# Kernel tuning notes

Hardware: AMD Instinct MI355X
Metric: run time of the kernel (lower is better)

Reference implementation:

```python
import jax, jax.numpy as jnp
import numpy as np

# Static segment boundaries: lengths [512,512,512] + remainder -> ranges below
SEG_RANGES = [(0, 512), (512, 1024), (1024, 1536), (1536, 2048)]

B, N, D, H = 8, 2048, 1024, 2048
NUM_SEG = len(SEG_RANGES)


def setup_inputs() -> dict:
    key = jax.random.key(0)
    k_x, k1, k2, k3 = jax.random.split(key, 4)
    scale_in = 1.0 / np.sqrt(D)
    scale_h = 1.0 / np.sqrt(H)
    return {
        "x": jax.random.normal(k_x, (B, N, D), dtype=jnp.float32),
        "w1": jax.random.normal(k1, (NUM_SEG, D, H), dtype=jnp.float32) * scale_in,
        "w3": jax.random.normal(k2, (NUM_SEG, D, H), dtype=jnp.float32) * scale_in,
        "w2": jax.random.normal(k3, (NUM_SEG, H, D), dtype=jnp.float32) * scale_h,
    }


def reference(x, w1, w3, w2):
    # Per-segment independent SwiGLU FFN: out_seg = (silu(x W1) * (x W3)) W2
    outs = []
    for i, (s, e) in enumerate(SEG_RANGES):
        seg = jax.lax.dynamic_slice_in_dim(x, s, e - s, axis=-2)  # [B, L_i, D]
        h = jax.nn.silu(jnp.einsum('bld,dh->blh', seg, w1[i])) \
            * jnp.einsum('bld,dh->blh', seg, w3[i])               # [B, L_i, H]
        outs.append(jnp.einsum('blh,hd->bld', h, w2[i]))          # [B, L_i, D]
    # Segments tile [0, N) exactly, so concat == the .at[s:e].set() scatter loop
    return jnp.concatenate(outs, axis=-2)
```

## Files before the change

kernel.cpp:

```cpp
#include <hip/hip_runtime.h>
#include <hip/hip_bf16.h>

typedef __bf16 bf16_t;
typedef __attribute__((ext_vector_type(8))) __bf16 bf16x8;
typedef __attribute__((ext_vector_type(4))) float f32x4;
typedef __attribute__((ext_vector_type(8))) unsigned short ushort8v;

#define MFMA16(a, b, c) __builtin_amdgcn_mfma_f32_16x16x32_bf16((a), (b), (c), 0, 0, 0)
#define BC8(x) __builtin_bit_cast(bf16x8, (x))

__device__ __forceinline__ unsigned short f2bf(float f) {
    bf16_t b = (bf16_t)f;
    return __builtin_bit_cast(unsigned short, b);
}

__device__ __forceinline__ void gload16(const void* g, void* l) {
    __builtin_amdgcn_global_load_lds(
        (const __attribute__((address_space(1))) void*)g,
        (__attribute__((address_space(3))) void*)l,
        16, 0, 0);
}

__global__ __launch_bounds__(256) void cvtx(const float* __restrict__ src,
                                            bf16_t* __restrict__ dst) {
    size_t i = ((size_t)blockIdx.x * 256 + threadIdx.x) * 8;
    f32x4 v0 = *(const f32x4*)(src + i);
    f32x4 v1 = *(const f32x4*)(src + i + 4);
    bf16x8 o;
    o[0] = (bf16_t)v0[0]; o[1] = (bf16_t)v0[1];
    o[2] = (bf16_t)v0[2]; o[3] = (bf16_t)v0[3];
    o[4] = (bf16_t)v1[0]; o[5] = (bf16_t)v1[1];
    o[6] = (bf16_t)v1[2]; o[7] = (bf16_t)v1[3];
    *(bf16x8*)(dst + i) = o;
}

__global__ __launch_bounds__(256) void transcvt64(const float* __restrict__ src,
                                                  unsigned short* __restrict__ dst,
                                                  int R, int C) {
    __shared__ __align__(16) unsigned short tile[64][66];
    size_t off = (size_t)blockIdx.z * R * C;
    const float* s = src + off;
    unsigned short* d = dst + off;
    int tr = blockIdx.y * 64, tc = blockIdx.x * 64;
    int tid = threadIdx.x;
    int lr = tid >> 4;
    int lc = (tid & 15) * 4;
#pragma unroll
    for (int p = 0; p < 4; ++p) {
        int r = p * 16 + lr;
        f32x4 v = *(const f32x4*)(s + (size_t)(tr + r) * C + tc + lc);
        tile[r][lc + 0] = f2bf(v[0]); tile[r][lc + 1] = f2bf(v[1]);
        tile[r][lc + 2] = f2bf(v[2]); tile[r][lc + 3] = f2bf(v[3]);
    }
    __syncthreads();
#pragma unroll
    for (int q = 0; q < 2; ++q) {
        int item = q * 256 + tid;
        int oc = item >> 3;
        int rb = (item & 7) * 8;
        ushort8v v;
#pragma unroll
        for (int t = 0; t < 8; ++t) v[t] = tile[rb + t][oc];
        *(ushort8v*)(d + (size_t)(tc + oc) * R + tr + rb) = v;
    }
}


#define PH_FENCE __builtin_amdgcn_sched_barrier(0)
#define LGKMN(n) { asm volatile("s_waitcnt lgkmcnt(" #n ")" ::: "memory"); \
                   __builtin_amdgcn_sched_barrier(0); }
#define VMW(n) asm volatile("s_waitcnt vmcnt(" #n ")" ::: "memory")
#define DSR(dst, a, OFF) asm volatile("ds_read_b128 %0, %1 " OFF : "=v"(dst) : "v"(a))

__global__ __launch_bounds__(512, 2) void gemm13(const bf16_t* __restrict__ Xb,
                                                 const bf16_t* __restrict__ W1t,
                                                 const bf16_t* __restrict__ W3t,
                                                 bf16_t* __restrict__ Hh,
                                                 int row_base) {
    const int K = 1024, N = 2048;
    int nwg = gridDim.x, id = blockIdx.x;
    if ((nwg & 7) == 0) id = (id & 7) * (nwg >> 3) + (id >> 3);
    int nbx = nwg >> 4;
    int bx = id % nbx, by = id / nbx;
    int row0 = bx * 256, col0 = by * 128;
    int seg = ((row_base + row0) & 2047) >> 9;
    const bf16_t* Ag  = Xb + (size_t)row0 * K;
    const bf16_t* B1g = W1t + ((size_t)seg * N + col0) * K;
    const bf16_t* B3g = W3t + ((size_t)seg * N + col0) * K;

    __shared__ __align__(16) bf16_t smem[65536];

    int tid = threadIdx.x, lane = tid & 63, w = tid >> 6;
    int wm = w >> 1, wn = w & 1;
    int quad = lane >> 4, l16 = lane & 15;

    int r0 = 2 * (tid >> 3) + ((tid >> 2) & 1);
    int c0 = (tid & 3) ^ ((tid >> 3) & 3);
    int offG  = r0 * K + c0 * 8;
    int offG2 = offG + 128 * K;

    int sigRd = ((l16 & 1) << 2) | (quad ^ ((l16 >> 1) & 3));
    int rdAB = ((wm * 32 + (l16 >> 1)) * 64 + sigRd * 8) * 2;
    int rdBB = ((wn * 32 + (l16 >> 1)) * 64 + sigRd * 8) * 2;

    f32x4 accU[4][4], accV[4][4];
    f32x4 z = {0.f, 0.f, 0.f, 0.f};
#pragma unroll
    for (int i = 0; i < 4; ++i)
#pragma unroll
        for (int j = 0; j < 4; ++j) { accU[i][j] = z; accV[i][j] = z; }

    f32x4 af[4], bU[4], bV[4];

#define STG13(slot, hh) { bf16_t* d_ = smem + (slot) * 16384; const int kg_ = (hh) * 32; \
    gload16(Ag + kg_ + offG,  d_ + tid * 8); \
    gload16(Ag + kg_ + offG2, d_ + 4096 + tid * 8); \
    gload16(B1g + kg_ + offG, d_ + 8192 + tid * 8); \
    gload16(B3g + kg_ + offG, d_ + 12288 + tid * 8); }

#define HALF13(slot, STG, WAIT) {                                               \
    PH_FENCE;                                                                   \
    STG;                                                                        \
    int aA_ = (slot) * 32768 + rdAB;                                            \
    int aB_ = (slot) * 32768 + rdBB;                                            \
    DSR(af[0], aA_, "offset:0");     DSR(af[1], aA_, "offset:1024");            \
    DSR(af[2], aA_, "offset:2048");  DSR(af[3], aA_, "offset:3072");            \
    DSR(bU[0], aB_, "offset:16384"); DSR(bU[1], aB_, "offset:17408");           \
    DSR(bU[2], aB_, "offset:18432"); DSR(bU[3], aB_, "offset:19456");           \
    DSR(bV[0], aB_, "offset:24576"); DSR(bV[1], aB_, "offset:25600");           \
    DSR(bV[2], aB_, "offset:26624"); DSR(bV[3], aB_, "offset:27648");           \
    LGKMN(4);                                                                   \
    __builtin_amdgcn_s_setprio(1);                                              \
    _Pragma("unroll")                                                           \
    for (int i_ = 0; i_ < 4; ++i_)                                              \
        _Pragma("unroll")                                                       \
        for (int j_ = 0; j_ < 4; ++j_)                                          \
            accU[i_][j_] = MFMA16(BC8(af[i_]), BC8(bU[j_]), accU[i_][j_]);      \
    __builtin_amdgcn_s_setprio(0);                                              \
    LGKMN(0);                                                                   \
    __builtin_amdgcn_s_setprio(1);                                              \
    _Pragma("unroll")                                                           \
    for (int i_ = 0; i_ < 4; ++i_)                                              \
        _Pragma("unroll")                                                       \
        for (int j_ = 0; j_ < 4; ++j_)                                          \
            accV[i_][j_] = MFMA16(BC8(af[i_]), BC8(bV[j_]), accV[i_][j_]);      \
    __builtin_amdgcn_s_setprio(0);                                              \
    WAIT;                                                                       \
    __builtin_amdgcn_s_barrier(); }

    STG13(0, 0); STG13(1, 1); STG13(2, 2);
    VMW(8);
    __builtin_amdgcn_s_barrier();

#pragma unroll 1
    for (int h = 0; h < 28; h += 4) {
        HALF13(0, STG13(3, h + 3), VMW(8));
        HALF13(1, STG13(0, h + 4), VMW(8));
        HALF13(2, STG13(1, h + 5), VMW(8));
        HALF13(3, STG13(2, h + 6), VMW(8));
    }
    HALF13(0, STG13(3, 31), VMW(8));
    HALF13(1, , VMW(4));
    HALF13(2, , VMW(0));
    HALF13(3, , );

    __syncthreads();
    bf16_t* Ct = smem;
#pragma unroll
    for (int i = 0; i < 4; ++i)
#pragma unroll
        for (int j = 0; j < 4; ++j) {
            int r = wm * 64 + i * 16 + quad * 4;
            int c = wn * 64 + j * 16 + l16;
#pragma unroll
            for (int t = 0; t < 4; ++t) {
                float u = accU[i][j][t];
                float v = accV[i][j][t];
                float h = (u / (1.f + __expf(-u))) * v;
                Ct[(r + t) * 136 + c] = (bf16_t)h;
            }
        }
    __syncthreads();
#pragma unroll
    for (int s = 0; s < 8; ++s) {
        int r = s * 32 + (tid >> 4);
        int cb = (tid & 15) * 8;
        bf16x8 v = *(const bf16x8*)(Ct + r * 136 + cb);
        *(bf16x8*)(Hh + (size_t)(row0 + r) * N + col0 + cb) = v;
    }
#undef HALF13
#undef STG13
}

__global__ __launch_bounds__(512, 2) void gemm2k(const bf16_t* __restrict__ Hh,
                                                 const bf16_t* __restrict__ W2t,
                                                 float* __restrict__ Outc,
                                                 int row_base) {
    const int K = 2048, N = 1024;
    int nwg = gridDim.x, id = blockIdx.x;
    if ((nwg & 7) == 0) id = (id & 7) * (nwg >> 3) + (id >> 3);
    int nbx = nwg >> 2;
    int bx = id % nbx, by = id / nbx;
    int row0 = bx * 256, col0 = by * 256;
    int seg = ((row_base + row0) & 2047) >> 9;
    const bf16_t* Ag = Hh + (size_t)row0 * K;
    const bf16_t* Bg = W2t + ((size_t)seg * N + col0) * K;

    __shared__ __align__(16) bf16_t smem[65536];

    int tid = threadIdx.x, lane = tid & 63, w = tid >> 6;
    int wm = w >> 2, wn = w & 3;
    int quad = lane >> 4, l16 = lane & 15;

    int r0 = 2 * (tid >> 3) + ((tid >> 2) & 1);
    int c0 = (tid & 3) ^ ((tid >> 3) & 3);
    int offG  = r0 * K + c0 * 8;
    int offG2 = offG + 128 * K;

    int sigRd = ((l16 & 1) << 2) | (quad ^ ((l16 >> 1) & 3));
    int rdAB = ((wm * 64 + (l16 >> 1)) * 64 + sigRd * 8) * 2;
    int rdBB = ((wn * 32 + (l16 >> 1)) * 64 + sigRd * 8) * 2;

    f32x4 acc[8][4];
    f32x4 z = {0.f, 0.f, 0.f, 0.f};
#pragma unroll
    for (int i = 0; i < 8; ++i)
#pragma unroll
        for (int j = 0; j < 4; ++j) acc[i][j] = z;

    f32x4 af[4], ag[4], bfr[4];

#define STG2(slot, hh) { bf16_t* d_ = smem + (slot) * 16384; const int kg_ = (hh) * 32; \
    gload16(Ag + kg_ + offG,  d_ + tid * 8); \
    gload16(Ag + kg_ + offG2, d_ + 4096 + tid * 8); \
    gload16(Bg + kg_ + offG,  d_ + 8192 + tid * 8); \
    gload16(Bg + kg_ + offG2, d_ + 12288 + tid * 8); }

#define HALF2(slot, STG, WAIT) {                                                \
    PH_FENCE;                                                                   \
    STG;                                                                        \
    int aA_ = (slot) * 32768 + rdAB;                                            \
    int aB_ = (slot) * 32768 + rdBB;                                            \
    DSR(af[0], aA_, "offset:0");      DSR(af[1], aA_, "offset:1024");           \
    DSR(af[2], aA_, "offset:2048");   DSR(af[3], aA_, "offset:3072");           \
    DSR(bfr[0], aB_, "offset:16384"); DSR(bfr[1], aB_, "offset:17408");         \
    DSR(bfr[2], aB_, "offset:18432"); DSR(bfr[3], aB_, "offset:19456");         \
    DSR(ag[0], aA_, "offset:4096");   DSR(ag[1], aA_, "offset:5120");           \
    DSR(ag[2], aA_, "offset:6144");   DSR(ag[3], aA_, "offset:7168");           \
    LGKMN(4);                                                                   \
    __builtin_amdgcn_s_setprio(1);                                              \
    _Pragma("unroll")                                                           \
    for (int i_ = 0; i_ < 4; ++i_)                                              \
        _Pragma("unroll")                                                       \
        for (int j_ = 0; j_ < 4; ++j_)                                          \
            acc[i_][j_] = MFMA16(BC8(af[i_]), BC8(bfr[j_]), acc[i_][j_]);       \
    __builtin_amdgcn_s_setprio(0);                                              \
    LGKMN(0);                                                                   \
    __builtin_amdgcn_s_setprio(1);                                              \
    _Pragma("unroll")                                                           \
    for (int i_ = 0; i_ < 4; ++i_)                                              \
        _Pragma("unroll")                                                       \
        for (int j_ = 0; j_ < 4; ++j_)                                          \
            acc[4 + i_][j_] = MFMA16(BC8(ag[i_]), BC8(bfr[j_]), acc[4 + i_][j_]); \
    __builtin_amdgcn_s_setprio(0);                                              \
    WAIT;                                                                       \
    __builtin_amdgcn_s_barrier(); }

    STG2(0, 0); STG2(1, 1); STG2(2, 2);
    VMW(8);
    __builtin_amdgcn_s_barrier();

#pragma unroll 1
    for (int h = 0; h < 60; h += 4) {
        HALF2(0, STG2(3, h + 3), VMW(8));
        HALF2(1, STG2(0, h + 4), VMW(8));
        HALF2(2, STG2(1, h + 5), VMW(8));
        HALF2(3, STG2(2, h + 6), VMW(8));
    }
    HALF2(0, STG2(3, 63), VMW(8));
    HALF2(1, , VMW(4));
    HALF2(2, , VMW(0));
    HALF2(3, , );

    __syncthreads();
    float* smemf = (float*)smem;
    for (int pass = 0; pass < 4; ++pass) {
        if (pass) __syncthreads();
        if (wm == (pass >> 1)) {
            int mq = pass & 1;
#pragma unroll
            for (int i = 0; i < 4; ++i)
#pragma unroll
                for (int j = 0; j < 4; ++j) {
                    int r = i * 16 + quad * 4;
                    int c = wn * 64 + j * 16 + l16;
#pragma unroll
                    for (int t = 0; t < 4; ++t)
                        smemf[(r + t) * 260 + c] = acc[mq * 4 + i][j][t];
                }
        }
        __syncthreads();
#pragma unroll
        for (int s = 0; s < 8; ++s) {
            int r = s * 8 + w;
            f32x4 v = *(const f32x4*)(smemf + r * 260 + lane * 4);
            *(f32x4*)(Outc + (size_t)(row0 + pass * 64 + r) * N + col0 + lane * 4) = v;
        }
    }
#undef HALF2
#undef STG2
}

extern "C" void kernel_launch(void* const* d_in, const int* in_sizes, int n_in,
                              void* d_out, int out_size, void* d_ws, size_t ws_size,
                              hipStream_t stream) {
    const float* x  = (const float*)d_in[0];
    const float* w1 = (const float*)d_in[1];
    const float* w3 = (const float*)d_in[2];
    const float* w2 = (const float*)d_in[3];
    float* out = (float*)d_out;

    const size_t WSEG = (size_t)4 * 1024 * 2048;
    bf16_t* w1t = (bf16_t*)d_ws;
    bf16_t* w3t = w1t + WSEG;
    bf16_t* w2t = w3t + WSEG;
    bf16_t* dyn = w2t + WSEG;

    transcvt64<<<dim3(32, 16, 4), 256, 0, stream>>>(w1, (unsigned short*)w1t, 1024, 2048);
    transcvt64<<<dim3(32, 16, 4), 256, 0, stream>>>(w3, (unsigned short*)w3t, 1024, 2048);
    transcvt64<<<dim3(16, 32, 4), 256, 0, stream>>>(w2, (unsigned short*)w2t, 2048, 1024);

    const int TOTAL_ROWS = 16384;
    size_t wbytes = 3 * WSEG * sizeof(bf16_t);
    size_t avail = (ws_size > wbytes) ? ws_size - wbytes : 0;
    int chunk_rows = TOTAL_ROWS;
    while (chunk_rows > 256 && (size_t)chunk_rows * 6144 > avail)
        chunk_rows >>= 1;

    for (int rb = 0; rb < TOTAL_ROWS; rb += chunk_rows) {
        bf16_t* Xb = dyn;
        bf16_t* Hh = dyn + (size_t)chunk_rows * 1024;
        cvtx<<<chunk_rows / 2, 256, 0, stream>>>(x + (size_t)rb * 1024, Xb);
        gemm13<<<(chunk_rows / 256) * 16, 512, 0, stream>>>(Xb, w1t, w3t, Hh, rb);
        gemm2k<<<(chunk_rows / 256) * 4, 512, 0, stream>>>(Hh, w2t, out + (size_t)rb * 1024, rb);
    }
}
```

Before: 400.3 us.

## Double-buffer LDS fragment registers to prefetch next stage during MFMAs

```diff
diff --git a/kernel.cpp b/kernel.cpp
--- a/kernel.cpp
+++ b/kernel.cpp
@@ -66,7 +66,6 @@
 }
 
 
-#define PH_FENCE __builtin_amdgcn_sched_barrier(0)
 #define LGKMN(n) { asm volatile("s_waitcnt lgkmcnt(" #n ")" ::: "memory"); \
                    __builtin_amdgcn_sched_barrier(0); }
 #define VMW(n) asm volatile("s_waitcnt vmcnt(" #n ")" ::: "memory")
@@ -110,7 +109,7 @@
 #pragma unroll
         for (int j = 0; j < 4; ++j) { accU[i][j] = z; accV[i][j] = z; }
 
-    f32x4 af[4], bU[4], bV[4];
+    f32x4 af[2][4], bU[2][4], bV[2][4];
 
 #define STG13(slot, hh) { bf16_t* d_ = smem + (slot) * 16384; const int kg_ = (hh) * 32; \
     gload16(Ag + kg_ + offG,  d_ + tid * 8); \
@@ -118,51 +117,52 @@
     gload16(B1g + kg_ + offG, d_ + 8192 + tid * 8); \
     gload16(B3g + kg_ + offG, d_ + 12288 + tid * 8); }
 
-#define HALF13(slot, STG, WAIT) {                                               \
-    PH_FENCE;                                                                   \
+#define RD13(slotN, BN) {                                                       \
+    int aA_ = (slotN) * 32768 + rdAB;                                           \
+    int aB_ = (slotN) * 32768 + rdBB;                                           \
+    DSR(af[BN][0], aA_, "offset:0");     DSR(af[BN][1], aA_, "offset:1024");    \
+    DSR(af[BN][2], aA_, "offset:2048");  DSR(af[BN][3], aA_, "offset:3072");    \
+    DSR(bU[BN][0], aB_, "offset:16384"); DSR(bU[BN][1], aB_, "offset:17408");   \
+    DSR(bU[BN][2], aB_, "offset:18432"); DSR(bU[BN][3], aB_, "offset:19456");   \
+    DSR(bV[BN][0], aB_, "offset:24576"); DSR(bV[BN][1], aB_, "offset:25600");   \
+    DSR(bV[BN][2], aB_, "offset:26624"); DSR(bV[BN][3], aB_, "offset:27648"); }
+
+#define HALF13(BC, RD, STG, WAIT) {                                             \
+    LGKMN(0);                                                                   \
+    RD;                                                                         \
     STG;                                                                        \
-    int aA_ = (slot) * 32768 + rdAB;                                            \
-    int aB_ = (slot) * 32768 + rdBB;                                            \
-    DSR(af[0], aA_, "offset:0");     DSR(af[1], aA_, "offset:1024");            \
-    DSR(af[2], aA_, "offset:2048");  DSR(af[3], aA_, "offset:3072");            \
-    DSR(bU[0], aB_, "offset:16384"); DSR(bU[1], aB_, "offset:17408");           \
-    DSR(bU[2], aB_, "offset:18432"); DSR(bU[3], aB_, "offset:19456");           \
-    DSR(bV[0], aB_, "offset:24576"); DSR(bV[1], aB_, "offset:25600");           \
-    DSR(bV[2], aB_, "offset:26624"); DSR(bV[3], aB_, "offset:27648");           \
-    LGKMN(4);                                                                   \
+    __builtin_amdgcn_sched_barrier(0);                                          \
     __builtin_amdgcn_s_setprio(1);                                              \
     _Pragma("unroll")                                                           \
     for (int i_ = 0; i_ < 4; ++i_)                                              \
         _Pragma("unroll")                                                       \
         for (int j_ = 0; j_ < 4; ++j_)                                          \
-            accU[i_][j_] = MFMA16(BC8(af[i_]), BC8(bU[j_]), accU[i_][j_]);      \
-    __builtin_amdgcn_s_setprio(0);                                              \
-    LGKMN(0);                                                                   \
-    __builtin_amdgcn_s_setprio(1);                                              \
+            accU[i_][j_] = MFMA16(BC8(af[BC][i_]), BC8(bU[BC][j_]), accU[i_][j_]); \
     _Pragma("unroll")                                                           \
     for (int i_ = 0; i_ < 4; ++i_)                                              \
         _Pragma("unroll")                                                       \
         for (int j_ = 0; j_ < 4; ++j_)                                          \
-            accV[i_][j_] = MFMA16(BC8(af[i_]), BC8(bV[j_]), accV[i_][j_]);      \
+            accV[i_][j_] = MFMA16(BC8(af[BC][i_]), BC8(bV[BC][j_]), accV[i_][j_]); \
     __builtin_amdgcn_s_setprio(0);                                              \
     WAIT;                                                                       \
     __builtin_amdgcn_s_barrier(); }
 
     STG13(0, 0); STG13(1, 1); STG13(2, 2);
-    VMW(8);
+    VMW(4);
     __builtin_amdgcn_s_barrier();
+    RD13(0, 0);
 
 #pragma unroll 1
     for (int h = 0; h < 28; h += 4) {
-        HALF13(0, STG13(3, h + 3), VMW(8));
-        HALF13(1, STG13(0, h + 4), VMW(8));
-        HALF13(2, STG13(1, h + 5), VMW(8));
-        HALF13(3, STG13(2, h + 6), VMW(8));
-    }
-    HALF13(0, STG13(3, 31), VMW(8));
-    HALF13(1, , VMW(4));
-    HALF13(2, , VMW(0));
-    HALF13(3, , );
+        HALF13(0, RD13(1, 1), STG13(3, h + 3), VMW(4));
+        HALF13(1, RD13(2, 0), STG13(0, h + 4), VMW(4));
+        HALF13(0 + 0, RD13(3, 1), STG13(1, h + 5), VMW(4));
+        HALF13(1, RD13(0, 0), STG13(2, h + 6), VMW(4));
+    }
+    HALF13(0, RD13(1, 1), STG13(3, 31), VMW(4));
+    HALF13(1, RD13(2, 0), , VMW(0));
+    HALF13(0, RD13(3, 1), , );
+    HALF13(1, , , );
 
     __syncthreads();
     bf16_t* Ct = smem;
@@ -189,6 +189,7 @@
         *(bf16x8*)(Hh + (size_t)(row0 + r) * N + col0 + cb) = v;
     }
 #undef HALF13
+#undef RD13
 #undef STG13
 }
 
@@ -228,7 +229,7 @@
 #pragma unroll
         for (int j = 0; j < 4; ++j) acc[i][j] = z;
 
-    f32x4 af[4], ag[4], bfr[4];
+    f32x4 af[2][4], ag[2][4], bfr[2][4];
 
 #define STG2(slot, hh) { bf16_t* d_ = smem + (slot) * 16384; const int kg_ = (hh) * 32; \
     gload16(Ag + kg_ + offG,  d_ + tid * 8); \
@@ -236,51 +237,52 @@
     gload16(Bg + kg_ + offG,  d_ + 8192 + tid * 8); \
     gload16(Bg + kg_ + offG2, d_ + 12288 + tid * 8); }
 
-#define HALF2(slot, STG, WAIT) {                                                \
-    PH_FENCE;                                                                   \
+#define RD2(slotN, BN) {                                                        \
+    int aA_ = (slotN) * 32768 + rdAB;                                           \
+    int aB_ = (slotN) * 32768 + rdBB;                                           \
+    DSR(af[BN][0], aA_, "offset:0");      DSR(af[BN][1], aA_, "offset:1024");   \
+    DSR(af[BN][2], aA_, "offset:2048");   DSR(af[BN][3], aA_, "offset:3072");   \
+    DSR(ag[BN][0], aA_, "offset:4096");   DSR(ag[BN][1], aA_, "offset:5120");   \
+    DSR(ag[BN][2], aA_, "offset:6144");   DSR(ag[BN][3], aA_, "offset:7168");   \
+    DSR(bfr[BN][0], aB_, "offset:16384"); DSR(bfr[BN][1], aB_, "offset:17408"); \
+    DSR(bfr[BN][2], aB_, "offset:18432"); DSR(bfr[BN][3], aB_, "offset:19456"); }
+
+#define HALF2(BC, RD, STG, WAIT) {                                              \
+    LGKMN(0);                                                                   \
+    RD;                                                                         \
     STG;                                                                        \
-    int aA_ = (slot) * 32768 + rdAB;                                            \
-    int aB_ = (slot) * 32768 + rdBB;                                            \
-    DSR(af[0], aA_, "offset:0");      DSR(af[1], aA_, "offset:1024");           \
-    DSR(af[2], aA_, "offset:2048");   DSR(af[3], aA_, "offset:3072");           \
-    DSR(bfr[0], aB_, "offset:16384"); DSR(bfr[1], aB_, "offset:17408");         \
-    DSR(bfr[2], aB_, "offset:18432"); DSR(bfr[3], aB_, "offset:19456");         \
-    DSR(ag[0], aA_, "offset:4096");   DSR(ag[1], aA_, "offset:5120");           \
-    DSR(ag[2], aA_, "offset:6144");   DSR(ag[3], aA_, "offset:7168");           \
-    LGKMN(4);                                                                   \
+    __builtin_amdgcn_sched_barrier(0);                                          \
     __builtin_amdgcn_s_setprio(1);                                              \
     _Pragma("unroll")                                                           \
     for (int i_ = 0; i_ < 4; ++i_)                                              \
         _Pragma("unroll")                                                       \
         for (int j_ = 0; j_ < 4; ++j_)                                          \
-            acc[i_][j_] = MFMA16(BC8(af[i_]), BC8(bfr[j_]), acc[i_][j_]);       \
-    __builtin_amdgcn_s_setprio(0);                                              \
-    LGKMN(0);                                                                   \
-    __builtin_amdgcn_s_setprio(1);                                              \
+            acc[i_][j_] = MFMA16(BC8(af[BC][i_]), BC8(bfr[BC][j_]), acc[i_][j_]); \
     _Pragma("unroll")                                                           \
     for (int i_ = 0; i_ < 4; ++i_)                                              \
         _Pragma("unroll")                                                       \
         for (int j_ = 0; j_ < 4; ++j_)                                          \
-            acc[4 + i_][j_] = MFMA16(BC8(ag[i_]), BC8(bfr[j_]), acc[4 + i_][j_]); \
+            acc[4 + i_][j_] = MFMA16(BC8(ag[BC][i_]), BC8(bfr[BC][j_]), acc[4 + i_][j_]); \
     __builtin_amdgcn_s_setprio(0);                                              \
     WAIT;                                                                       \
     __builtin_amdgcn_s_barrier(); }
 
     STG2(0, 0); STG2(1, 1); STG2(2, 2);
-    VMW(8);
+    VMW(4);
     __builtin_amdgcn_s_barrier();
+    RD2(0, 0);
 
 #pragma unroll 1
     for (int h = 0; h < 60; h += 4) {
-        HALF2(0, STG2(3, h + 3), VMW(8));
-        HALF2(1, STG2(0, h + 4), VMW(8));
-        HALF2(2, STG2(1, h + 5), VMW(8));
-        HALF2(3, STG2(2, h + 6), VMW(8));
-    }
-    HALF2(0, STG2(3, 63), VMW(8));
-    HALF2(1, , VMW(4));
-    HALF2(2, , VMW(0));
-    HALF2(3, , );
+        HALF2(0, RD2(1, 1), STG2(3, h + 3), VMW(4));
+        HALF2(1, RD2(2, 0), STG2(0, h + 4), VMW(4));
+        HALF2(0, RD2(3, 1), STG2(1, h + 5), VMW(4));
+        HALF2(1, RD2(0, 0), STG2(2, h + 6), VMW(4));
+    }
+    HALF2(0, RD2(1, 1), STG2(3, 63), VMW(4));
+    HALF2(1, RD2(2, 0), , VMW(0));
+    HALF2(0, RD2(3, 1), , );
+    HALF2(1, , , );
 
     __syncthreads();
     float* smemf = (float*)smem;
@@ -308,6 +310,7 @@
         }
     }
 #undef HALF2
+#undef RD2
 #undef STG2
 }
 
```

Measured after the change: 592.1 us. +47.9%, slower.

## Split each K-step into two barrier-separated phases interleaving loads and MFMA

Applied to the files above, without the earlier changes.

```diff
diff --git a/kernel.cpp b/kernel.cpp
--- a/kernel.cpp
+++ b/kernel.cpp
@@ -66,7 +66,6 @@
 }
 
 
-#define PH_FENCE __builtin_amdgcn_sched_barrier(0)
 #define LGKMN(n) { asm volatile("s_waitcnt lgkmcnt(" #n ")" ::: "memory"); \
                    __builtin_amdgcn_sched_barrier(0); }
 #define VMW(n) asm volatile("s_waitcnt vmcnt(" #n ")" ::: "memory")
@@ -112,24 +111,23 @@
 
     f32x4 af[4], bU[4], bV[4];
 
-#define STG13(slot, hh) { bf16_t* d_ = smem + (slot) * 16384; const int kg_ = (hh) * 32; \
+#define STGA13(slot, hh) { bf16_t* d_ = smem + (slot) * 16384; const int kg_ = (hh) * 32; \
     gload16(Ag + kg_ + offG,  d_ + tid * 8); \
-    gload16(Ag + kg_ + offG2, d_ + 4096 + tid * 8); \
+    gload16(Ag + kg_ + offG2, d_ + 4096 + tid * 8); }
+#define STGB13(slot, hh) { bf16_t* d_ = smem + (slot) * 16384; const int kg_ = (hh) * 32; \
     gload16(B1g + kg_ + offG, d_ + 8192 + tid * 8); \
     gload16(B3g + kg_ + offG, d_ + 12288 + tid * 8); }
 
-#define HALF13(slot, STG, WAIT) {                                               \
-    PH_FENCE;                                                                   \
-    STG;                                                                        \
+#define PHA13(slot, STG) {                                                      \
     int aA_ = (slot) * 32768 + rdAB;                                            \
     int aB_ = (slot) * 32768 + rdBB;                                            \
     DSR(af[0], aA_, "offset:0");     DSR(af[1], aA_, "offset:1024");            \
     DSR(af[2], aA_, "offset:2048");  DSR(af[3], aA_, "offset:3072");            \
     DSR(bU[0], aB_, "offset:16384"); DSR(bU[1], aB_, "offset:17408");           \
     DSR(bU[2], aB_, "offset:18432"); DSR(bU[3], aB_, "offset:19456");           \
-    DSR(bV[0], aB_, "offset:24576"); DSR(bV[1], aB_, "offset:25600");           \
-    DSR(bV[2], aB_, "offset:26624"); DSR(bV[3], aB_, "offset:27648");           \
-    LGKMN(4);                                                                   \
+    STG;                                                                        \
+    __builtin_amdgcn_s_barrier();                                               \
+    LGKMN(0);                                                                   \
     __builtin_amdgcn_s_setprio(1);                                              \
     _Pragma("unroll")                                                           \
     for (int i_ = 0; i_ < 4; ++i_)                                              \
@@ -137,6 +135,15 @@
         for (int j_ = 0; j_ < 4; ++j_)                                          \
             accU[i_][j_] = MFMA16(BC8(af[i_]), BC8(bU[j_]), accU[i_][j_]);      \
     __builtin_amdgcn_s_setprio(0);                                              \
+    __builtin_amdgcn_s_barrier(); }
+
+#define PHB13(slot, STG, WAIT) {                                                \
+    int aB_ = (slot) * 32768 + rdBB;                                            \
+    DSR(bV[0], aB_, "offset:24576"); DSR(bV[1], aB_, "offset:25600");           \
+    DSR(bV[2], aB_, "offset:26624"); DSR(bV[3], aB_, "offset:27648");           \
+    STG;                                                                        \
+    WAIT;                                                                       \
+    __builtin_amdgcn_s_barrier();                                               \
     LGKMN(0);                                                                   \
     __builtin_amdgcn_s_setprio(1);                                              \
     _Pragma("unroll")                                                           \
@@ -145,24 +152,25 @@
         for (int j_ = 0; j_ < 4; ++j_)                                          \
             accV[i_][j_] = MFMA16(BC8(af[i_]), BC8(bV[j_]), accV[i_][j_]);      \
     __builtin_amdgcn_s_setprio(0);                                              \
-    WAIT;                                                                       \
     __builtin_amdgcn_s_barrier(); }
 
-    STG13(0, 0); STG13(1, 1); STG13(2, 2);
+    STGA13(0, 0); STGB13(0, 0);
+    STGA13(1, 1); STGB13(1, 1);
+    STGA13(2, 2); STGB13(2, 2);
     VMW(8);
     __builtin_amdgcn_s_barrier();
 
 #pragma unroll 1
     for (int h = 0; h < 28; h += 4) {
-        HALF13(0, STG13(3, h + 3), VMW(8));
-        HALF13(1, STG13(0, h + 4), VMW(8));
-        HALF13(2, STG13(1, h + 5), VMW(8));
-        HALF13(3, STG13(2, h + 6), VMW(8));
-    }
-    HALF13(0, STG13(3, 31), VMW(8));
-    HALF13(1, , VMW(4));
-    HALF13(2, , VMW(0));
-    HALF13(3, , );
+        PHA13(0, STGA13(3, h + 3)); PHB13(0, STGB13(3, h + 3), VMW(8));
+        PHA13(1, STGA13(0, h + 4)); PHB13(1, STGB13(0, h + 4), VMW(8));
+        PHA13(2, STGA13(1, h + 5)); PHB13(2, STGB13(1, h + 5), VMW(8));
+        PHA13(3, STGA13(2, h + 6)); PHB13(3, STGB13(2, h + 6), VMW(8));
+    }
+    PHA13(0, STGA13(3, 31)); PHB13(0, STGB13(3, 31), VMW(8));
+    PHA13(1, );              PHB13(1, , VMW(4));
+    PHA13(2, );              PHB13(2, , VMW(0));
+    PHA13(3, );              PHB13(3, , );
 
     __syncthreads();
     bf16_t* Ct = smem;
@@ -188,8 +196,10 @@
         bf16x8 v = *(const bf16x8*)(Ct + r * 136 + cb);
         *(bf16x8*)(Hh + (size_t)(row0 + r) * N + col0 + cb) = v;
     }
-#undef HALF13
-#undef STG13
+#undef PHA13
+#undef PHB13
+#undef STGA13
+#undef STGB13
 }
 
 __global__ __launch_bounds__(512, 2) void gemm2k(const bf16_t* __restrict__ Hh,
@@ -230,24 +240,23 @@
 
     f32x4 af[4], ag[4], bfr[4];
 
-#define STG2(slot, hh) { bf16_t* d_ = smem + (slot) * 16384; const int kg_ = (hh) * 32; \
+#define STGA2(slot, hh) { bf16_t* d_ = smem + (slot) * 16384; const int kg_ = (hh) * 32; \
     gload16(Ag + kg_ + offG,  d_ + tid * 8); \
-    gload16(Ag + kg_ + offG2, d_ + 4096 + tid * 8); \
+    gload16(Ag + kg_ + offG2, d_ + 4096 + tid * 8); }
+#define STGB2(slot, hh) { bf16_t* d_ = smem + (slot) * 16384; const int kg_ = (hh) * 32; \
     gload16(Bg + kg_ + offG,  d_ + 8192 + tid * 8); \
     gload16(Bg + kg_ + offG2, d_ + 12288 + tid * 8); }
 
-#define HALF2(slot, STG, WAIT) {                                                \
-    PH_FENCE;                                                                   \
-    STG;                                                                        \
+#define PHA2(slot, STG) {                                                       \
     int aA_ = (slot) * 32768 + rdAB;                                            \
     int aB_ = (slot) * 32768 + rdBB;                                            \
     DSR(af[0], aA_, "offset:0");      DSR(af[1], aA_, "offset:1024");           \
     DSR(af[2], aA_, "offset:2048");   DSR(af[3], aA_, "offset:3072");           \
     DSR(bfr[0], aB_, "offset:16384"); DSR(bfr[1], aB_, "offset:17408");         \
     DSR(bfr[2], aB_, "offset:18432"); DSR(bfr[3], aB_, "offset:19456");         \
-    DSR(ag[0], aA_, "offset:4096");   DSR(ag[1], aA_, "offset:5120");           \
-    DSR(ag[2], aA_, "offset:6144");   DSR(ag[3], aA_, "offset:7168");           \
-    LGKMN(4);                                                                   \
+    STG;                                                                        \
+    __builtin_amdgcn_s_barrier();                                               \
+    LGKMN(0);                                                                   \
     __builtin_amdgcn_s_setprio(1);                                              \
     _Pragma("unroll")                                                           \
     for (int i_ = 0; i_ < 4; ++i_)                                              \
@@ -255,6 +264,15 @@
         for (int j_ = 0; j_ < 4; ++j_)                                          \
             acc[i_][j_] = MFMA16(BC8(af[i_]), BC8(bfr[j_]), acc[i_][j_]);       \
     __builtin_amdgcn_s_setprio(0);                                              \
+    __builtin_amdgcn_s_barrier(); }
+
+#define PHB2(slot, STG, WAIT) {                                                 \
+    int aA_ = (slot) * 32768 + rdAB;                                            \
+    DSR(ag[0], aA_, "offset:4096");   DSR(ag[1], aA_, "offset:5120");           \
+    DSR(ag[2], aA_, "offset:6144");   DSR(ag[3], aA_, "offset:7168");           \
+    STG;                                                                        \
+    WAIT;                                                                       \
+    __builtin_amdgcn_s_barrier();                                               \
     LGKMN(0);                                                                   \
     __builtin_amdgcn_s_setprio(1);                                              \
     _Pragma("unroll")                                                           \
@@ -263,24 +281,25 @@
         for (int j_ = 0; j_ < 4; ++j_)                                          \
             acc[4 + i_][j_] = MFMA16(BC8(ag[i_]), BC8(bfr[j_]), acc[4 + i_][j_]); \
     __builtin_amdgcn_s_setprio(0);                                              \
-    WAIT;                                                                       \
     __builtin_amdgcn_s_barrier(); }
 
-    STG2(0, 0); STG2(1, 1); STG2(2, 2);
+    STGA2(0, 0); STGB2(0, 0);
+    STGA2(1, 1); STGB2(1, 1);
+    STGA2(2, 2); STGB2(2, 2);
     VMW(8);
     __builtin_amdgcn_s_barrier();
 
 #pragma unroll 1
     for (int h = 0; h < 60; h += 4) {
-        HALF2(0, STG2(3, h + 3), VMW(8));
-        HALF2(1, STG2(0, h + 4), VMW(8));
-        HALF2(2, STG2(1, h + 5), VMW(8));
-        HALF2(3, STG2(2, h + 6), VMW(8));
-    }
-    HALF2(0, STG2(3, 63), VMW(8));
-    HALF2(1, , VMW(4));
-    HALF2(2, , VMW(0));
-    HALF2(3, , );
+        PHA2(0, STGA2(3, h + 3)); PHB2(0, STGB2(3, h + 3), VMW(8));
+        PHA2(1, STGA2(0, h + 4)); PHB2(1, STGB2(0, h + 4), VMW(8));
+        PHA2(2, STGA2(1, h + 5)); PHB2(2, STGB2(1, h + 5), VMW(8));
+        PHA2(3, STGA2(2, h + 6)); PHB2(3, STGB2(2, h + 6), VMW(8));
+    }
+    PHA2(0, STGA2(3, 63)); PHB2(0, STGB2(3, 63), VMW(8));
+    PHA2(1, );             PHB2(1, , VMW(4));
+    PHA2(2, );             PHB2(2, , VMW(0));
+    PHA2(3, );             PHB2(3, , );
 
     __syncthreads();
     float* smemf = (float*)smem;
@@ -307,8 +326,10 @@
             *(f32x4*)(Outc + (size_t)(row0 + pass * 64 + r) * N + col0 + lane * 4) = v;
         }
     }
-#undef HALF2
-#undef STG2
+#undef PHA2
+#undef PHB2
+#undef STGA2
+#undef STGB2
 }
 
 extern "C" void kernel_launch(void* const* d_in, const int* in_sizes, int n_in,
```

Result: no change. 403.0 us (+0.7%).

## Shrink GEMM workgroups to 256 threads with 128-row tiles and triple buffering

Applied to the files above, without the earlier changes.

```diff
diff --git a/kernel.cpp b/kernel.cpp
--- a/kernel.cpp
+++ b/kernel.cpp
@@ -66,13 +66,12 @@
 }
 
 
-#define PH_FENCE __builtin_amdgcn_sched_barrier(0)
 #define LGKMN(n) { asm volatile("s_waitcnt lgkmcnt(" #n ")" ::: "memory"); \
                    __builtin_amdgcn_sched_barrier(0); }
 #define VMW(n) asm volatile("s_waitcnt vmcnt(" #n ")" ::: "memory")
 #define DSR(dst, a, OFF) asm volatile("ds_read_b128 %0, %1 " OFF : "=v"(dst) : "v"(a))
 
-__global__ __launch_bounds__(512, 2) void gemm13(const bf16_t* __restrict__ Xb,
+__global__ __launch_bounds__(256, 2) void gemm13(const bf16_t* __restrict__ Xb,
                                                  const bf16_t* __restrict__ W1t,
                                                  const bf16_t* __restrict__ W3t,
                                                  bf16_t* __restrict__ Hh,
@@ -82,13 +81,13 @@
     if ((nwg & 7) == 0) id = (id & 7) * (nwg >> 3) + (id >> 3);
     int nbx = nwg >> 4;
     int bx = id % nbx, by = id / nbx;
-    int row0 = bx * 256, col0 = by * 128;
+    int row0 = bx * 128, col0 = by * 128;
     int seg = ((row_base + row0) & 2047) >> 9;
     const bf16_t* Ag  = Xb + (size_t)row0 * K;
     const bf16_t* B1g = W1t + ((size_t)seg * N + col0) * K;
     const bf16_t* B3g = W3t + ((size_t)seg * N + col0) * K;
 
-    __shared__ __align__(16) bf16_t smem[65536];
+    __shared__ __align__(16) bf16_t smem[36864];
 
     int tid = threadIdx.x, lane = tid & 63, w = tid >> 6;
     int wm = w >> 1, wn = w & 1;
@@ -96,8 +95,7 @@
 
     int r0 = 2 * (tid >> 3) + ((tid >> 2) & 1);
     int c0 = (tid & 3) ^ ((tid >> 3) & 3);
-    int offG  = r0 * K + c0 * 8;
-    int offG2 = offG + 128 * K;
+    int offG = r0 * K + c0 * 8;
 
     int sigRd = ((l16 & 1) << 2) | (quad ^ ((l16 >> 1) & 3));
     int rdAB = ((wm * 32 + (l16 >> 1)) * 64 + sigRd * 8) * 2;
@@ -112,23 +110,24 @@
 
     f32x4 af[4], bU[4], bV[4];
 
-#define STG13(slot, hh) { bf16_t* d_ = smem + (slot) * 16384; const int kg_ = (hh) * 32; \
-    gload16(Ag + kg_ + offG,  d_ + tid * 8); \
-    gload16(Ag + kg_ + offG2, d_ + 4096 + tid * 8); \
-    gload16(B1g + kg_ + offG, d_ + 8192 + tid * 8); \
-    gload16(B3g + kg_ + offG, d_ + 12288 + tid * 8); }
+#define STG13(slot, hh) { bf16_t* d_ = smem + (slot) * 12288; const int kg_ = (hh) * 32; \
+    gload16(Ag + kg_ + offG,          d_ + tid * 8); \
+    gload16(Ag + kg_ + offG + 65536,  d_ + 2048 + tid * 8); \
+    gload16(B1g + kg_ + offG,         d_ + 4096 + tid * 8); \
+    gload16(B1g + kg_ + offG + 65536, d_ + 6144 + tid * 8); \
+    gload16(B3g + kg_ + offG,         d_ + 8192 + tid * 8); \
+    gload16(B3g + kg_ + offG + 65536, d_ + 10240 + tid * 8); }
 
 #define HALF13(slot, STG, WAIT) {                                               \
-    PH_FENCE;                                                                   \
+    int aA_ = (slot) * 24576 + rdAB;                                            \
+    int aB_ = (slot) * 24576 + 8192 + rdBB;                                     \
+    DSR(af[0], aA_, "offset:0");    DSR(af[1], aA_, "offset:1024");             \
+    DSR(af[2], aA_, "offset:2048"); DSR(af[3], aA_, "offset:3072");             \
+    DSR(bU[0], aB_, "offset:0");    DSR(bU[1], aB_, "offset:1024");             \
+    DSR(bU[2], aB_, "offset:2048"); DSR(bU[3], aB_, "offset:3072");             \
+    DSR(bV[0], aB_, "offset:8192"); DSR(bV[1], aB_, "offset:9216");             \
+    DSR(bV[2], aB_, "offset:10240");DSR(bV[3], aB_, "offset:11264");            \
     STG;                                                                        \
-    int aA_ = (slot) * 32768 + rdAB;                                            \
-    int aB_ = (slot) * 32768 + rdBB;                                            \
-    DSR(af[0], aA_, "offset:0");     DSR(af[1], aA_, "offset:1024");            \
-    DSR(af[2], aA_, "offset:2048");  DSR(af[3], aA_, "offset:3072");            \
-    DSR(bU[0], aB_, "offset:16384"); DSR(bU[1], aB_, "offset:17408");           \
-    DSR(bU[2], aB_, "offset:18432"); DSR(bU[3], aB_, "offset:19456");           \
-    DSR(bV[0], aB_, "offset:24576"); DSR(bV[1], aB_, "offset:25600");           \
-    DSR(bV[2], aB_, "offset:26624"); DSR(bV[3], aB_, "offset:27648");           \
     LGKMN(4);                                                                   \
     __builtin_amdgcn_s_setprio(1);                                              \
     _Pragma("unroll")                                                           \
@@ -148,21 +147,21 @@
     WAIT;                                                                       \
     __builtin_amdgcn_s_barrier(); }
 
-    STG13(0, 0); STG13(1, 1); STG13(2, 2);
-    VMW(8);
+    STG13(0, 0); STG13(1, 1);
+    VMW(6);
     __builtin_amdgcn_s_barrier();
 
 #pragma unroll 1
-    for (int h = 0; h < 28; h += 4) {
-        HALF13(0, STG13(3, h + 3), VMW(8));
-        HALF13(1, STG13(0, h + 4), VMW(8));
-        HALF13(2, STG13(1, h + 5), VMW(8));
-        HALF13(3, STG13(2, h + 6), VMW(8));
-    }
-    HALF13(0, STG13(3, 31), VMW(8));
-    HALF13(1, , VMW(4));
-    HALF13(2, , VMW(0));
-    HALF13(3, , );
+    for (int h = 0; h < 27; h += 3) {
+        HALF13(0, STG13(2, h + 2), VMW(6));
+        HALF13(1, STG13(0, h + 3), VMW(6));
+        HALF13(2, STG13(1, h + 4), VMW(6));
+    }
+    HALF13(0, STG13(2, 29), VMW(6));
+    HALF13(1, STG13(0, 30), VMW(6));
+    HALF13(2, STG13(1, 31), VMW(6));
+    HALF13(0, , VMW(0));
+    HALF13(1, , );
 
     __syncthreads();
     bf16_t* Ct = smem;
@@ -183,7 +182,7 @@
     __syncthreads();
 #pragma unroll
     for (int s = 0; s < 8; ++s) {
-        int r = s * 32 + (tid >> 4);
+        int r = s * 16 + (tid >> 4);
         int cb = (tid & 15) * 8;
         bf16x8 v = *(const bf16x8*)(Ct + r * 136 + cb);
         *(bf16x8*)(Hh + (size_t)(row0 + r) * N + col0 + cb) = v;
@@ -192,7 +191,7 @@
 #undef STG13
 }
 
-__global__ __launch_bounds__(512, 2) void gemm2k(const bf16_t* __restrict__ Hh,
+__global__ __launch_bounds__(256, 2) void gemm2k(const bf16_t* __restrict__ Hh,
                                                  const bf16_t* __restrict__ W2t,
                                                  float* __restrict__ Outc,
                                                  int row_base) {
@@ -201,52 +200,52 @@
     if ((nwg & 7) == 0) id = (id & 7) * (nwg >> 3) + (id >> 3);
     int nbx = nwg >> 2;
     int bx = id % nbx, by = id / nbx;
-    int row0 = bx * 256, col0 = by * 256;
+    int row0 = bx * 128, col0 = by * 256;
     int seg = ((row_base + row0) & 2047) >> 9;
     const bf16_t* Ag = Hh + (size_t)row0 * K;
     const bf16_t* Bg = W2t + ((size_t)seg * N + col0) * K;
 
-    __shared__ __align__(16) bf16_t smem[65536];
+    __shared__ __align__(16) bf16_t smem[36864];
 
     int tid = threadIdx.x, lane = tid & 63, w = tid >> 6;
-    int wm = w >> 2, wn = w & 3;
+    int wm = w >> 1, wn = w & 1;
     int quad = lane >> 4, l16 = lane & 15;
 
     int r0 = 2 * (tid >> 3) + ((tid >> 2) & 1);
     int c0 = (tid & 3) ^ ((tid >> 3) & 3);
-    int offG  = r0 * K + c0 * 8;
-    int offG2 = offG + 128 * K;
+    int offG = r0 * K + c0 * 8;
 
     int sigRd = ((l16 & 1) << 2) | (quad ^ ((l16 >> 1) & 3));
-    int rdAB = ((wm * 64 + (l16 >> 1)) * 64 + sigRd * 8) * 2;
-    int rdBB = ((wn * 32 + (l16 >> 1)) * 64 + sigRd * 8) * 2;
-
-    f32x4 acc[8][4];
+    int rdAB = ((wm * 32 + (l16 >> 1)) * 64 + sigRd * 8) * 2;
+    int rdBB = ((wn * 64 + (l16 >> 1)) * 64 + sigRd * 8) * 2;
+
+    f32x4 acc[4][8];
     f32x4 z = {0.f, 0.f, 0.f, 0.f};
 #pragma unroll
-    for (int i = 0; i < 8; ++i)
-#pragma unroll
-        for (int j = 0; j < 4; ++j) acc[i][j] = z;
-
-    f32x4 af[4], ag[4], bfr[4];
-
-#define STG2(slot, hh) { bf16_t* d_ = smem + (slot) * 16384; const int kg_ = (hh) * 32; \
-    gload16(Ag + kg_ + offG,  d_ + tid * 8); \
-    gload16(Ag + kg_ + offG2, d_ + 4096 + tid * 8); \
-    gload16(Bg + kg_ + offG,  d_ + 8192 + tid * 8); \
-    gload16(Bg + kg_ + offG2, d_ + 12288 + tid * 8); }
+    for (int i = 0; i < 4; ++i)
+#pragma unroll
+        for (int j = 0; j < 8; ++j) acc[i][j] = z;
+
+    f32x4 af[4], bfr[8];
+
+#define STG2(slot, hh) { bf16_t* d_ = smem + (slot) * 12288; const int kg_ = (hh) * 32; \
+    gload16(Ag + kg_ + offG,           d_ + tid * 8); \
+    gload16(Ag + kg_ + offG + 131072,  d_ + 2048 + tid * 8); \
+    gload16(Bg + kg_ + offG,           d_ + 4096 + tid * 8); \
+    gload16(Bg + kg_ + offG + 131072,  d_ + 6144 + tid * 8); \
+    gload16(Bg + kg_ + offG + 262144,  d_ + 8192 + tid * 8); \
+    gload16(Bg + kg_ + offG + 393216,  d_ + 10240 + tid * 8); }
 
 #define HALF2(slot, STG, WAIT) {                                                \
-    PH_FENCE;                                                                   \
+    int aA_ = (slot) * 24576 + rdAB;                                            \
+    int aB_ = (slot) * 24576 + 8192 + rdBB;                                     \
+    DSR(af[0], aA_, "offset:0");     DSR(af[1], aA_, "offset:1024");            \
+    DSR(af[2], aA_, "offset:2048");  DSR(af[3], aA_, "offset:3072");            \
+    DSR(bfr[0], aB_, "offset:0");    DSR(bfr[1], aB_, "offset:1024");           \
+    DSR(bfr[2], aB_, "offset:2048"); DSR(bfr[3], aB_, "offset:3072");           \
+    DSR(bfr[4], aB_, "offset:4096"); DSR(bfr[5], aB_, "offset:5120");           \
+    DSR(bfr[6], aB_, "offset:6144"); DSR(bfr[7], aB_, "offset:7168");           \
     STG;                                                                        \
-    int aA_ = (slot) * 32768 + rdAB;                                            \
-    int aB_ = (slot) * 32768 + rdBB;                                            \
-    DSR(af[0], aA_, "offset:0");      DSR(af[1], aA_, "offset:1024");           \
-    DSR(af[2], aA_, "offset:2048");   DSR(af[3], aA_, "offset:3072");           \
-    DSR(bfr[0], aB_, "offset:16384"); DSR(bfr[1], aB_, "offset:17408");         \
-    DSR(bfr[2], aB_, "offset:18432"); DSR(bfr[3], aB_, "offset:19456");         \
-    DSR(ag[0], aA_, "offset:4096");   DSR(ag[1], aA_, "offset:5120");           \
-    DSR(ag[2], aA_, "offset:6144");   DSR(ag[3], aA_, "offset:7168");           \
     LGKMN(4);                                                                   \
     __builtin_amdgcn_s_setprio(1);                                              \
     _Pragma("unroll")                                                           \
@@ -261,50 +260,49 @@
     for (int i_ = 0; i_ < 4; ++i_)                                              \
         _Pragma("unroll")                                                       \
         for (int j_ = 0; j_ < 4; ++j_)                                          \
-            acc[4 + i_][j_] = MFMA16(BC8(ag[i_]), BC8(bfr[j_]), acc[4 + i_][j_]); \
+            acc[i_][4 + j_] = MFMA16(BC8(af[i_]), BC8(bfr[4 + j_]), acc[i_][4 + j_]); \
     __builtin_amdgcn_s_setprio(0);                                              \
     WAIT;                                                                       \
     __builtin_amdgcn_s_barrier(); }
 
-    STG2(0, 0); STG2(1, 1); STG2(2, 2);
-    VMW(8);
+    STG2(0, 0); STG2(1, 1);
+    VMW(6);
     __builtin_amdgcn_s_barrier();
 
 #pragma unroll 1
-    for (int h = 0; h < 60; h += 4) {
-        HALF2(0, STG2(3, h + 3), VMW(8));
-        HALF2(1, STG2(0, h + 4), VMW(8));
-        HALF2(2, STG2(1, h + 5), VMW(8));
-        HALF2(3, STG2(2, h + 6), VMW(8));
-    }
-    HALF2(0, STG2(3, 63), VMW(8));
-    HALF2(1, , VMW(4));
+    for (int h = 0; h < 60; h += 3) {
+        HALF2(0, STG2(2, h + 2), VMW(6));
+        HALF2(1, STG2(0, h + 3), VMW(6));
+        HALF2(2, STG2(1, h + 4), VMW(6));
+    }
+    HALF2(0, STG2(2, 62), VMW(6));
+    HALF2(1, STG2(0, 63), VMW(6));
     HALF2(2, , VMW(0));
-    HALF2(3, , );
+    HALF2(0, , );
 
     __syncthreads();
     float* smemf = (float*)smem;
-    for (int pass = 0; pass < 4; ++pass) {
+    for (int pass = 0; pass < 2; ++pass) {
         if (pass) __syncthreads();
-        if (wm == (pass >> 1)) {
-            int mq = pass & 1;
+        if (wm == pass) {
 #pragma unroll
             for (int i = 0; i < 4; ++i)
 #pragma unroll
-                for (int j = 0; j < 4; ++j) {
+                for (int j = 0; j < 8; ++j) {
                     int r = i * 16 + quad * 4;
-                    int c = wn * 64 + j * 16 + l16;
+                    int c = wn * 128 + j * 16 + l16;
 #pragma unroll
                     for (int t = 0; t < 4; ++t)
-                        smemf[(r + t) * 260 + c] = acc[mq * 4 + i][j][t];
+                        smemf[(r + t) * 260 + c] = acc[i][j][t];
                 }
         }
         __syncthreads();
 #pragma unroll
-        for (int s = 0; s < 8; ++s) {
-            int r = s * 8 + w;
-            f32x4 v = *(const f32x4*)(smemf + r * 260 + lane * 4);
-            *(f32x4*)(Outc + (size_t)(row0 + pass * 64 + r) * N + col0 + lane * 4) = v;
+        for (int s = 0; s < 16; ++s) {
+            int r = s * 4 + (tid >> 6);
+            int cb = (tid & 63) * 4;
+            f32x4 v = *(const f32x4*)(smemf + r * 260 + cb);
+            *(f32x4*)(Outc + (size_t)(row0 + pass * 64 + r) * N + col0 + cb) = v;
         }
     }
 #undef HALF2
@@ -334,14 +332,14 @@
     size_t wbytes = 3 * WSEG * sizeof(bf16_t);
     size_t avail = (ws_size > wbytes) ? ws_size - wbytes : 0;
     int chunk_rows = TOTAL_ROWS;
-    while (chunk_rows > 256 && (size_t)chunk_rows * 6144 > avail)
+    while (chunk_rows > 128 && (size_t)chunk_rows * 6144 > avail)
         chunk_rows >>= 1;
 
     for (int rb = 0; rb < TOTAL_ROWS; rb += chunk_rows) {
         bf16_t* Xb = dyn;
         bf16_t* Hh = dyn + (size_t)chunk_rows * 1024;
         cvtx<<<chunk_rows / 2, 256, 0, stream>>>(x + (size_t)rb * 1024, Xb);
-        gemm13<<<(chunk_rows / 256) * 16, 512, 0, stream>>>(Xb, w1t, w3t, Hh, rb);
-        gemm2k<<<(chunk_rows / 256) * 4, 512, 0, stream>>>(Hh, w2t, out + (size_t)rb * 1024, rb);
-    }
-}
+        gemm13<<<(chunk_rows / 128) * 16, 256, 0, stream>>>(Xb, w1t, w3t, Hh, rb);
+        gemm2k<<<(chunk_rows / 128) * 4, 256, 0, stream>>>(Hh, w2t, out + (size_t)rb * 1024, rb);
+    }
+}
```

After: 401.5 us. Within noise of the previous version (+0.3%).
